# Optimization experiments

Measured on AMD Instinct MI355X. Metric: run time of the kernel, lower is better.

## Reference

```python
import jax, jax.numpy as jnp
import numpy as np

B, T, TM = 4, 1024, 1500
D_MODEL, D_FFN, H, D_HEAD, D_MEM = 1024, 4096, 16, 64, 1024
EPS = 1e-5


def layernorm(x, g):
    m = jnp.mean(x, axis=-1, keepdims=True)
    xc = x - m
    v = jnp.mean(xc * xc, axis=-1, keepdims=True)
    return xc * jax.lax.rsqrt(v + EPS) * g


def setup_inputs() -> dict:
    key = jax.random.key(0)
    ks = jax.random.split(key, 12)
    s = lambda fan_in: 1.0 / np.sqrt(fan_in)
    return {
        "x": jax.random.normal(ks[0], (B, T, D_MODEL), jnp.float32),
        "encoder_output": jax.random.normal(ks[1], (B, TM, D_MEM), jnp.float32),
        "encoder_mask": jax.random.randint(ks[2], (B, TM), 0, 2).astype(bool),
        "w_qkv": jax.random.normal(ks[3], (D_MODEL, 3 * H * D_HEAD), jnp.float32) * s(D_MODEL),
        "w_o_sa": jax.random.normal(ks[4], (H * D_HEAD, D_MODEL), jnp.float32) * s(H * D_HEAD),
        "w_q": jax.random.normal(ks[5], (D_MODEL, H * D_HEAD), jnp.float32) * s(D_MODEL),
        "w_kv": jax.random.normal(ks[6], (D_MEM, 2 * H * D_HEAD), jnp.float32) * s(D_MEM),
        "w_o_xa": jax.random.normal(ks[7], (H * D_HEAD, D_MODEL), jnp.float32) * s(H * D_HEAD),
        "w_ff1": jax.random.normal(ks[8], (D_MODEL, D_FFN), jnp.float32) * s(D_MODEL),
        "w_ff2": jax.random.normal(ks[9], (D_FFN, D_MODEL), jnp.float32) * s(D_FFN),
        "g_sa": jnp.ones((D_MODEL,), jnp.float32),
        "g_xaq": jnp.ones((D_MODEL,), jnp.float32),
        "g_xam": jnp.ones((D_MEM,), jnp.float32),
        "g_ff": jnp.ones((D_MODEL,), jnp.float32),
    }


def reference(x, encoder_output, encoder_mask, w_qkv, w_o_sa, w_q, w_kv, w_o_xa,
              w_ff1, w_ff2, g_sa, g_xaq, g_xam, g_ff):
    b, t, _ = x.shape
    scale = D_HEAD ** -0.5

    # ---- causal self-attention ----
    residual = x
    xn = layernorm(x, g_sa)
    qkv = (xn @ w_qkv).reshape(b, t, 3, H, D_HEAD)
    q, k, v = qkv[:, :, 0], qkv[:, :, 1], qkv[:, :, 2]  # (B,T,H,D)
    scores = jnp.einsum('bqhd,bkhd->bhqk', q, k) * scale
    causal = jnp.tril(jnp.ones((t, t), x.dtype))
    scores = scores + (1.0 - causal) * -1e9
    attn = jax.nn.softmax(scores, axis=-1)
    sa = jnp.einsum('bhqk,bkhd->bqhd', attn, v).reshape(b, t, H * D_HEAD)
    x = residual + sa @ w_o_sa

    # ---- cross-attention ----
    residual = x
    qn = layernorm(x, g_xaq)
    mn = layernorm(encoder_output, g_xam)
    tq, tm = t, mn.shape[1]
    qx = (qn @ w_q).reshape(b, tq, H, D_HEAD)
    kvx = (mn @ w_kv).reshape(b, tm, 2, H, D_HEAD)
    kx, vx = kvx[:, :, 0], kvx[:, :, 1]
    xs = jnp.einsum('bqhd,bkhd->bhqk', qx, kx) * scale
    xs = jnp.where(encoder_mask[:, None, None, :], xs, -jnp.inf)
    xattn = jax.nn.softmax(xs, axis=-1)
    xa = jnp.einsum('bhqk,bkhd->bqhd', xattn, vx).reshape(b, tq, H * D_HEAD)
    x = residual + xa @ w_o_xa

    # ---- pointwise FFN (kernel_size=1 conv == linear) ----
    residual = x
    h = layernorm(x, g_ff)
    h = jax.nn.gelu(h @ w_ff1, approximate=True) @ w_ff2
    x = residual + h
    return (x, k, v)
```

## Files before the change

### kernel.cpp

```cpp
#include <hip/hip_runtime.h>
#include <hip/hip_bf16.h>
#include <cstdint>
#include <cstddef>


typedef __attribute__((ext_vector_type(4))) float f32x4;
typedef __attribute__((ext_vector_type(8))) short s8v;
typedef __attribute__((ext_vector_type(2))) unsigned uint2v;

#define DEVI __device__ __forceinline__

DEVI short f2bf(float f) {
  union { float f; unsigned u; } x; x.f = f;
  unsigned r = x.u + 0x7fffu + ((x.u >> 16) & 1u);
  return (short)(r >> 16);
}
DEVI unsigned cvtpk_bf2(float lo, float hi) {
  unsigned r;
  asm("v_cvt_pk_bf16_f32 %0, %1, %2" : "=v"(r) : "v"(lo), "v"(hi));
  return r;
}
DEVI float fexp2(float x) {
  float r;
  asm("v_exp_f32 %0, %1" : "=v"(r) : "v"(x));
  return r;
}
DEVI float fmax3(float a, float b, float c) {
  float r;
  asm("v_max3_f32 %0, %1, %2, %3" : "=v"(r) : "v"(a), "v"(b), "v"(c));
  return r;
}
DEVI float bpermf(int srclane, float v) {
  union { float f; int i; } x; x.f = v;
  x.i = __builtin_amdgcn_ds_bpermute(srclane << 2, x.i);
  return x.f;
}
DEVI void gload_lds16(const void* g, void* l) {
  __builtin_amdgcn_global_load_lds((const __attribute__((address_space(1))) void*)g,
                                   (__attribute__((address_space(3))) void*)l,
                                   16, 0, 0);
}

DEVI void xcd_swizzle(int& bx, int& by) {
  int gx = gridDim.x, gy = gridDim.y;
  int nxy = gx * gy, chunk = nxy >> 3;
  int orig = blockIdx.y * gx + blockIdx.x;
  int gid = (orig & 7) * chunk + (orig >> 3);
  int full = gy << 3, nfull = gx >> 3, lim = nfull * full;
  if (gid < lim) {
    int band = gid / full, r = gid - band * full;
    bx = (band << 3) + (r & 7);
    by = r >> 3;
  } else {
    int r = gid - lim, w = gx - (nfull << 3);
    bx = (nfull << 3) + r % w;
    by = r / w;
  }
}

__global__ __launch_bounds__(256) void k_prep(
    const float* __restrict__ wqkv, const float* __restrict__ wosa,
    const float* __restrict__ wq,   const float* __restrict__ wkv,
    const float* __restrict__ woxa, const float* __restrict__ wff1,
    const float* __restrict__ wff2,
    short* __restrict__ wqkv_t, short* __restrict__ wosa_t,
    short* __restrict__ wq_t,   short* __restrict__ wkv_t,
    short* __restrict__ woxa_t, short* __restrict__ wff1_t,
    short* __restrict__ wff2_t,
    const int* __restrict__ mask, unsigned long long* __restrict__ mbits) {
  int id = blockIdx.x;
  const float* w; short* wt; int K, N, tx, r;
  if (id < 3072)       { w = wqkv; wt = wqkv_t; K = 1024; N = 3072; tx = 96;  r = id; }
  else if (id < 4096)  { w = wosa; wt = wosa_t; K = 1024; N = 1024; tx = 32;  r = id - 3072; }
  else if (id < 5120)  { w = wq;   wt = wq_t;   K = 1024; N = 1024; tx = 32;  r = id - 4096; }
  else if (id < 7168)  { w = wkv;  wt = wkv_t;  K = 1024; N = 2048; tx = 64;  r = id - 5120; }
  else if (id < 8192)  { w = woxa; wt = woxa_t; K = 1024; N = 1024; tx = 32;  r = id - 7168; }
  else if (id < 12288) { w = wff1; wt = wff1_t; K = 1024; N = 4096; tx = 128; r = id - 8192; }
  else if (id < 16384) { w = wff2; wt = wff2_t; K = 4096; N = 1024; tx = 32;  r = id - 12288; }
  else {
    int t = threadIdx.x;
    if (t < 96) {
      int b = t / 24, wd = t % 24;
      unsigned long long v = 0;
      const int* mb = mask + (size_t)b * 1500;
      for (int j = 0; j < 64; j++) {
        int k = wd * 64 + j;
        if (k < 1500 && mb[k]) v |= (1ull << j);
      }
      mbits[b * 24 + wd] = v;
    }
    return;
  }
  __shared__ float tile[32][33];
  int n0 = (r % tx) * 32, k0 = (r / tx) * 32;
  int t = threadIdx.x;
  int row = t >> 3, c4 = (t & 7) * 4;
  *(f32x4*)&tile[row][c4] = *(const f32x4*)(w + (size_t)(k0 + row) * N + n0 + c4);
  __syncthreads();
  float v0 = tile[c4 + 0][row], v1 = tile[c4 + 1][row];
  float v2 = tile[c4 + 2][row], v3 = tile[c4 + 3][row];
  uint2v o = {cvtpk_bf2(v0, v1), cvtpk_bf2(v2, v3)};
  *(uint2v*)(wt + (size_t)(n0 + row) * K + k0 + c4) = o;
}

__global__ __launch_bounds__(256) void k_vtrans(
    const short* __restrict__ src, int srs, int coff,
    short* __restrict__ dst, int T, int Tp) {
  __shared__ short tile[32][72];
  int bh = blockIdx.y, b = bh >> 4, h = bh & 15;
  int t0 = blockIdx.x * 32;
  const short* sB = src + (size_t)b * T * srs + coff + h * 64;
  short* dB = dst + (size_t)bh * 64 * Tp;
  int t = threadIdx.x;
  int r = t >> 3, c = (t & 7) * 8;
  int tr = t0 + r; if (tr > T - 1) tr = T - 1;
  *(s8v*)&tile[r][c] = *(const s8v*)(sB + (size_t)tr * srs + c);
  __syncthreads();
  int d = t & 63, ch = t >> 6;
  s8v o;
#pragma unroll
  for (int j = 0; j < 8; j++) o[j] = tile[ch * 8 + j][d];
  *(s8v*)(dB + (size_t)d * Tp + t0 + ch * 8) = o;
}

__global__ __launch_bounds__(256) void k_ln2(
    const float* __restrict__ x, const float* __restrict__ gx,
    short* __restrict__ ox,
    const float* __restrict__ e, const float* __restrict__ ge,
    short* __restrict__ oe) {
  int id = blockIdx.x;
  const float* src; const float* g; short* dst; int row;
  if (id < 4096) { src = x; g = gx; dst = ox; row = id; }
  else           { src = e; g = ge; dst = oe; row = id - 4096; }
  const float* xr = src + (size_t)row * 1024;
  int t = threadIdx.x, wid = t >> 6, lane = t & 63;
  f32x4 v = ((const f32x4*)xr)[t];
  float s = v[0] + v[1] + v[2] + v[3];
#pragma unroll
  for (int m = 32; m >= 1; m >>= 1) s += __shfl_xor(s, m);
  __shared__ float red[4];
  if (lane == 0) red[wid] = s;
  __syncthreads();
  float mean = (red[0] + red[1] + red[2] + red[3]) * (1.f / 1024.f);
  float q = 0.f;
#pragma unroll
  for (int i = 0; i < 4; i++) { v[i] -= mean; q += v[i] * v[i]; }
#pragma unroll
  for (int m = 32; m >= 1; m >>= 1) q += __shfl_xor(q, m);
  __syncthreads();
  if (lane == 0) red[wid] = q;
  __syncthreads();
  float var = (red[0] + red[1] + red[2] + red[3]) * (1.f / 1024.f);
  float rs = rsqrtf(var + 1e-5f);
  f32x4 gv = ((const f32x4*)g)[t];
  uint2v w = {cvtpk_bf2(v[0] * rs * gv[0], v[1] * rs * gv[1]),
              cvtpk_bf2(v[2] * rs * gv[2], v[3] * rs * gv[3])};
  *(uint2v*)(dst + (size_t)row * 1024 + t * 4) = w;
}

template <bool F32OUT, bool BF16OUT>
__global__ __launch_bounds__(256) void k_gemm3(
    const short* __restrict__ A, const short* __restrict__ Bt,
    float* __restrict__ Cf, short* __restrict__ Cb,
    int M, int N, int K, int lda, int ldb) {
  __shared__ short As[128 * 64];
  __shared__ short Bs[128 * 64];
  int z = blockIdx.z;
  A += (size_t)z * K;
  Bt += (size_t)z * K;
  if (F32OUT) Cf += (size_t)z * (size_t)M * N;

  int bx, by;
  xcd_swizzle(bx, by);
  int am = bx * 128, bn = by * 128;

  int t = threadIdx.x, wid = t >> 6, lane = t & 63;
  int la = lane & 15, lb = lane >> 4;
  int wr = wid >> 1, wc = wid & 1;

  const short* gp[8];
  int dof[8];
#pragma unroll
  for (int l = 0; l < 8; l++) {
    int cl = (l & 3) * 256 + t;
    int row = cl >> 3, g = cl & 7;
    int col = (g ^ (row & 7)) << 3;
    if (l < 4) {
      int ar = am + row; if (ar > M - 1) ar = M - 1;
      gp[l] = A + (size_t)ar * lda + col;
    } else {
      gp[l] = Bt + (size_t)(bn + row) * ldb + col;
    }
    dof[l] = ((l & 3) * 256 + wid * 64) * 8;
  }

  int aOff[4], bOff[4];
#pragma unroll
  for (int m = 0; m < 4; m++) {
    int r = wr * 64 + m * 16 + la;
    aOff[m] = r * 64 + ((lb ^ (r & 7)) << 3);
  }
#pragma unroll
  for (int n = 0; n < 4; n++) {
    int r = wc * 64 + n * 16 + la;
    bOff[n] = r * 64 + ((lb ^ (r & 7)) << 3);
  }

  f32x4 acc[4][4];
#pragma unroll
  for (int m = 0; m < 4; m++)
#pragma unroll
    for (int n = 0; n < 4; n++) acc[m][n] = (f32x4){0.f, 0.f, 0.f, 0.f};

  int nk = K >> 6;
  for (int ks = 0; ks < nk; ++ks) {
#pragma unroll
    for (int l = 0; l < 4; l++) { gload_lds16(gp[l], As + dof[l]); gp[l] += 64; }
#pragma unroll
    for (int l = 4; l < 8; l++) { gload_lds16(gp[l], Bs + dof[l]); gp[l] += 64; }
    __syncthreads();
#pragma unroll
    for (int kk = 0; kk < 2; kk++) {
      s8v af[4], bfg[4];
#pragma unroll
      for (int m = 0; m < 4; m++)
        af[m] = *(const s8v*)(As + (aOff[m] ^ (kk << 5)));
#pragma unroll
      for (int n = 0; n < 4; n++)
        bfg[n] = *(const s8v*)(Bs + (bOff[n] ^ (kk << 5)));
#pragma unroll
      for (int m = 0; m < 4; m++)
#pragma unroll
        for (int n = 0; n < 4; n++)
          acc[m][n] = __builtin_amdgcn_mfma_f32_16x16x32_bf16(af[m], bfg[n], acc[m][n], 0, 0, 0);
    }
    __syncthreads();
  }

#pragma unroll
  for (int m = 0; m < 4; m++) {
    int rb = am + wr * 64 + m * 16 + lb * 4;
#pragma unroll
    for (int n = 0; n < 4; n++) {
      int col = bn + wc * 64 + n * 16 + la;
#pragma unroll
      for (int j = 0; j < 4; j++) {
        int r = rb + j;
        if (r < M) {
          float v = acc[m][n][j];
          if (F32OUT) Cf[(size_t)r * N + col] = v;
          if (BF16OUT) Cb[(size_t)r * N + col] = f2bf(v);
        }
      }
    }
  }
}

template <bool GELU_, bool F32OUT, bool BF16OUT, bool KV>
__global__ __launch_bounds__(512) void k_gemm4(
    const short* __restrict__ A, const short* __restrict__ Bt,
    float* __restrict__ Cf, short* __restrict__ Cb,
    float* __restrict__ okv, int M, int N, int K, int lda, int ldb) {
  __shared__ short As[128 * 64];
  __shared__ short Bs[256 * 64];
  int z = blockIdx.z;
  A += (size_t)z * K;
  Bt += (size_t)z * K;
  if (F32OUT) Cf += (size_t)z * (size_t)M * N;

  int bx, by;
  xcd_swizzle(bx, by);
  int am = bx * 128, bn = by * 256;

  int t = threadIdx.x, wid = t >> 6, lane = t & 63;
  int la = lane & 15, lb = lane >> 4;
  int wr = wid >> 2, wc = wid & 3;

  const short* gpA[2]; const short* gpB[4];
  int dofA[2], dofB[4];
#pragma unroll
  for (int l = 0; l < 2; l++) {
    int c = l * 512 + t;
    int row = c >> 3, g = c & 7;
    int ar = am + row; if (ar > M - 1) ar = M - 1;
    gpA[l] = A + (size_t)ar * lda + ((g ^ (row & 7)) << 3);
    dofA[l] = (l * 512 + wid * 64) * 8;
  }
#pragma unroll
  for (int l = 0; l < 4; l++) {
    int c = l * 512 + t;
    int row = c >> 3, g = c & 7;
    gpB[l] = Bt + (size_t)(bn + row) * ldb + ((g ^ (row & 7)) << 3);
    dofB[l] = (l * 512 + wid * 64) * 8;
  }

  int aOff[4], bOff[4];
#pragma unroll
  for (int m = 0; m < 4; m++) {
    int r = wr * 64 + m * 16 + la;
    aOff[m] = r * 64 + ((lb ^ (r & 7)) << 3);
  }
#pragma unroll
  for (int n = 0; n < 4; n++) {
    int r = wc * 64 + n * 16 + la;
    bOff[n] = r * 64 + ((lb ^ (r & 7)) << 3);
  }

  f32x4 acc[4][4];
#pragma unroll
  for (int m = 0; m < 4; m++)
#pragma unroll
    for (int n = 0; n < 4; n++) acc[m][n] = (f32x4){0.f, 0.f, 0.f, 0.f};

  int nk = K >> 6;
  for (int ks = 0; ks < nk; ++ks) {
#pragma unroll
    for (int l = 0; l < 2; l++) { gload_lds16(gpA[l], As + dofA[l]); gpA[l] += 64; }
#pragma unroll
    for (int l = 0; l < 4; l++) { gload_lds16(gpB[l], Bs + dofB[l]); gpB[l] += 64; }
    __syncthreads();
#pragma unroll
    for (int kk = 0; kk < 2; kk++) {
      s8v af[4], bfg[4];
#pragma unroll
      for (int m = 0; m < 4; m++)
        af[m] = *(const s8v*)(As + (aOff[m] ^ (kk << 5)));
#pragma unroll
      for (int n = 0; n < 4; n++)
        bfg[n] = *(const s8v*)(Bs + (bOff[n] ^ (kk << 5)));
#pragma unroll
      for (int m = 0; m < 4; m++)
#pragma unroll
        for (int n = 0; n < 4; n++)
          acc[m][n] = __builtin_amdgcn_mfma_f32_16x16x32_bf16(af[m], bfg[n], acc[m][n], 0, 0, 0);
    }
    __syncthreads();
  }

#pragma unroll
  for (int m = 0; m < 4; m++) {
    int rb = am + wr * 64 + m * 16 + lb * 4;
#pragma unroll
    for (int n = 0; n < 4; n++) {
      int col = bn + wc * 64 + n * 16 + la;
#pragma unroll
      for (int j = 0; j < 4; j++) {
        int r = rb + j;
        if (r < M) {
          float v = acc[m][n][j];
          if (GELU_) {
            float u = v;
            float y = 0.7978845608f * u * (1.f + 0.044715f * u * u);
            float e = fexp2(fminf(y * 2.88539008f, 80.f));
            float th = (e - 1.f) * __builtin_amdgcn_rcpf(e + 1.f);
            v = 0.5f * u * (1.f + th);
          }
          if (F32OUT) Cf[(size_t)r * N + col] = v;
          if (BF16OUT) Cb[(size_t)r * N + col] = f2bf(v);
          if (KV) {
            if (col >= 2048)
              okv[(size_t)4096 * 1024 + (size_t)r * 1024 + (col - 2048)] = v;
            else if (col >= 1024)
              okv[(size_t)r * 1024 + (col - 1024)] = v;
          }
        }
      }
    }
  }
}

__global__ __launch_bounds__(256) void k_red2b(
    const f32x4* __restrict__ p, short* __restrict__ outb, int n) {
  int i = blockIdx.x * 256 + threadIdx.x;
  f32x4 v = p[i] + p[i + (size_t)n];
  uint2v w = {cvtpk_bf2(v[0], v[1]), cvtpk_bf2(v[2], v[3])};
  *(uint2v*)(outb + (size_t)i * 4) = w;
}

__global__ __launch_bounds__(256) void k_red4(
    const f32x4* __restrict__ p, const f32x4* __restrict__ res,
    float* __restrict__ outf, int n) {
  int i = blockIdx.x * 256 + threadIdx.x;
  f32x4 v = res[i] + ((p[i] + p[i + (size_t)n]) +
                      (p[i + 2 * (size_t)n] + p[i + 3 * (size_t)n]));
  ((f32x4*)outf)[i] = v;
}

__global__ __launch_bounds__(256) void k_red2ln(
    const f32x4* __restrict__ p, const f32x4* __restrict__ res,
    float* __restrict__ xout, short* __restrict__ nout,
    const float* __restrict__ g, int n) {
  int row = blockIdx.x;
  int t = threadIdx.x, wid = t >> 6, lane = t & 63;
  size_t i = (size_t)row * 256 + t;
  f32x4 v = res[i] + (p[i] + p[i + (size_t)n]);
  ((f32x4*)xout)[i] = v;
  float s = v[0] + v[1] + v[2] + v[3];
#pragma unroll
  for (int m = 32; m >= 1; m >>= 1) s += __shfl_xor(s, m);
  __shared__ float red[4];
  if (lane == 0) red[wid] = s;
  __syncthreads();
  float mean = (red[0] + red[1] + red[2] + red[3]) * (1.f / 1024.f);
  float q = 0.f;
#pragma unroll
  for (int k = 0; k < 4; k++) { v[k] -= mean; q += v[k] * v[k]; }
#pragma unroll
  for (int m = 32; m >= 1; m >>= 1) q += __shfl_xor(q, m);
  __syncthreads();
  if (lane == 0) red[wid] = q;
  __syncthreads();
  float var = (red[0] + red[1] + red[2] + red[3]) * (1.f / 1024.f);
  float rs = rsqrtf(var + 1e-5f);
  f32x4 gv = ((const f32x4*)g)[t];
  uint2v w = {cvtpk_bf2(v[0] * rs * gv[0], v[1] * rs * gv[1]),
              cvtpk_bf2(v[2] * rs * gv[2], v[3] * rs * gv[3])};
  *(uint2v*)(nout + (size_t)row * 1024 + t * 4) = w;
}

template <bool CAUSAL>
__global__ __launch_bounds__(512) void k_attn4(
    const short* __restrict__ qbuf, int qrs,
    const short* __restrict__ kbuf, int krs,
    const short* __restrict__ vT, int vts,
    short* __restrict__ obuf, int ors,
    const unsigned long long* __restrict__ mbits, int mwords,
    int Tq, int Tk, float scale) {
  __shared__ short Ks[64 * 64];
  __shared__ short Vs[64 * 64];
  __shared__ short Ps[8 * 1024];
  int lid = blockIdx.y * gridDim.x + blockIdx.x;
  int rest = lid >> 3;
  int bh = (lid & 7) * 8 + (rest & 7);
  int qsel = rest >> 3;
  int b = bh >> 4, h = bh & 15;
  int t = threadIdx.x, wid = t >> 6, lane = t & 63;
  int la = lane & 15, lb = lane >> 4;
  float lscale = scale * 1.44269504f;

  const short* qB = qbuf + (size_t)b * Tq * qrs + h * 64;
  const short* kB = kbuf + (size_t)b * Tk * krs + h * 64;
  const short* vB = vT + (size_t)bh * 64 * vts;
  char* Pw = (char*)(Ps + wid * 1024);

  int sr = t >> 3, scol = (t & 7) * 8;
  int swz = sr * 64 + (scol ^ ((sr & 7) << 3));

  int nsup = CAUSAL ? 2 : 1;
  for (int s = 0; s < nsup; s++) {
    int st = CAUSAL ? (s ? 7 - qsel : qsel) : qsel;
    int q0 = st * 128 + wid * 16;
    int nkt = CAUSAL ? 2 * st + 2 : (Tk + 63) >> 6;
    int lastkt = CAUSAL ? (q0 >> 6) : nkt - 1;

    s8v qf[2];
#pragma unroll
    for (int kk = 0; kk < 2; kk++)
      qf[kk] = *(const s8v*)(qB + (size_t)(q0 + la) * qrs + kk * 32 + lb * 8);

    f32x4 accO[4];
#pragma unroll
    for (int n = 0; n < 4; n++) accO[n] = (f32x4){0.f, 0.f, 0.f, 0.f};
    float m = -1e30f, l = 0.f;

    s8v krg, vrg;
    {
      int tk = sr; if (tk > Tk - 1) tk = Tk - 1;
      krg = *(const s8v*)(kB + (size_t)tk * krs + scol);
      vrg = *(const s8v*)(vB + (size_t)sr * vts + scol);
    }

    for (int kt = 0; kt < nkt; kt++) {
      int kb0 = kt << 6;
      __syncthreads();
      *(s8v*)&Ks[swz] = krg;
      *(s8v*)&Vs[swz] = vrg;
      __syncthreads();
      if (kt + 1 < nkt) {
        int kb = kb0 + 64;
        int tk = kb + sr; if (tk > Tk - 1) tk = Tk - 1;
        krg = *(const s8v*)(kB + (size_t)tk * krs + scol);
        vrg = *(const s8v*)(vB + (size_t)sr * vts + kb + scol);
      }
      if (kt > lastkt) continue;

      bool needMask;
      unsigned long long wm = ~0ull;
      if (CAUSAL) {
        needMask = (kt == lastkt);
      } else {
        wm = mbits[(size_t)b * mwords + kt];
        needMask = (wm != ~0ull);
      }

      float sc[4][4];
      __builtin_amdgcn_s_setprio(1);
#pragma unroll
      for (int n = 0; n < 4; n++) {
        f32x4 a = (f32x4){0.f, 0.f, 0.f, 0.f};
#pragma unroll
        for (int kk = 0; kk < 2; kk++) {
          s8v kf = *(const s8v*)&Ks[(n * 16 + la) * 64 +
                                    ((kk * 32 + lb * 8) ^ ((la & 7) << 3))];
          a = __builtin_amdgcn_mfma_f32_16x16x32_bf16(kf, qf[kk], a, 0, 0, 0);
        }
        if (needMask) {
#pragma unroll
          for (int j = 0; j < 4; j++) {
            int ki = n * 16 + lb * 4 + j;
            bool ok = CAUSAL ? (kb0 + ki <= q0 + la) : (((wm >> ki) & 1ull) != 0);
            sc[n][j] = ok ? a[j] : -1e30f;
          }
        } else {
#pragma unroll
          for (int j = 0; j < 4; j++) sc[n][j] = a[j];
        }
      }
      __builtin_amdgcn_s_setprio(0);

      float rn[4];
#pragma unroll
      for (int n = 0; n < 4; n++)
        rn[n] = fmaxf(fmax3(sc[n][0], sc[n][1], sc[n][2]), sc[n][3]);
      float tm = fmaxf(fmax3(rn[0], rn[1], rn[2]), rn[3]);
      tm = fmaxf(tm, __shfl_xor(tm, 16));
      tm = fmaxf(tm, __shfl_xor(tm, 32));
      tm = fmaxf(tm * lscale, -1e4f);

      bool skip = __all(tm - m <= 10.f);
      float alpha = 1.f;
      if (!skip) {
        float mn_ = fmaxf(m, tm);
        alpha = fexp2(m - mn_);
        m = mn_;
      }
      float nm = -m;

      unsigned W[4][2];
      float ps = 0.f;
#pragma unroll
      for (int n = 0; n < 4; n++) {
        float p0 = fexp2(__builtin_fmaf(sc[n][0], lscale, nm));
        float p1 = fexp2(__builtin_fmaf(sc[n][1], lscale, nm));
        float p2 = fexp2(__builtin_fmaf(sc[n][2], lscale, nm));
        float p3 = fexp2(__builtin_fmaf(sc[n][3], lscale, nm));
        ps += (p0 + p1) + (p2 + p3);
        W[n][0] = cvtpk_bf2(p0, p1);
        W[n][1] = cvtpk_bf2(p2, p3);
      }
      ps += __shfl_xor(ps, 16);
      ps += __shfl_xor(ps, 32);
      l = l * alpha + ps;

      if (!skip) {
#pragma unroll
        for (int j = 0; j < 4; j++) {
          float aj = bpermf(lb * 20 + j, alpha);
#pragma unroll
          for (int n = 0; n < 4; n++) accO[n][j] *= aj;
        }
      }

#pragma unroll
      for (int n = 0; n < 4; n++) {
        uint2v w2 = {W[n][0], W[n][1]};
        *(uint2v*)(Pw + ((la * 128 + n * 32 + lb * 8) ^ ((la & 7) << 4))) = w2;
      }
      __builtin_amdgcn_s_setprio(1);
#pragma unroll
      for (int kk = 0; kk < 2; kk++) {
        s8v pa = *(const s8v*)(Pw + ((la * 128 + kk * 64 + lb * 16) ^ ((la & 7) << 4)));
#pragma unroll
        for (int n = 0; n < 4; n++) {
          s8v vf = *(const s8v*)&Vs[(n * 16 + la) * 64 +
                                    ((kk * 32 + lb * 8) ^ ((la & 7) << 3))];
          accO[n] = __builtin_amdgcn_mfma_f32_16x16x32_bf16(pa, vf, accO[n], 0, 0, 0);
        }
      }
      __builtin_amdgcn_s_setprio(0);
    }

#pragma unroll
    for (int j = 0; j < 4; j++) {
      float lj = bpermf(lb * 20 + j, l);
      float inv = 1.f / lj;
      int r = q0 + lb * 4 + j;
#pragma unroll
      for (int n = 0; n < 4; n++)
        obuf[(size_t)(b * Tq + r) * ors + h * 64 + n * 16 + la] = f2bf(accO[n][j] * inv);
    }
  }
}

extern "C" void kernel_launch(void* const* d_in, const int* in_sizes, int n_in,
                              void* d_out, int out_size, void* d_ws, size_t ws_size,
                              hipStream_t stream) {
  (void)in_sizes; (void)n_in; (void)out_size; (void)ws_size;
  const float* x      = (const float*)d_in[0];
  const float* enc    = (const float*)d_in[1];
  const int*   mask   = (const int*)d_in[2];
  const float* w_qkv  = (const float*)d_in[3];
  const float* w_o_sa = (const float*)d_in[4];
  const float* w_q    = (const float*)d_in[5];
  const float* w_kv   = (const float*)d_in[6];
  const float* w_o_xa = (const float*)d_in[7];
  const float* w_ff1  = (const float*)d_in[8];
  const float* w_ff2  = (const float*)d_in[9];
  const float* g_sa   = (const float*)d_in[10];
  const float* g_xaq  = (const float*)d_in[11];
  const float* g_xam  = (const float*)d_in[12];
  const float* g_ff   = (const float*)d_in[13];

  float* out_x = (float*)d_out;
  float* out_k = out_x + (size_t)4096 * 1024;

  char* ws = (char*)d_ws;
  size_t off = 0;
  auto alloc = [&](size_t bytes) -> void* {
    void* p = ws + off;
    off += (bytes + 255) & ~(size_t)255;
    return p;
  };
  short* wqkv_t = (short*)alloc((size_t)3072 * 1024 * 2);
  short* wosa_t = (short*)alloc((size_t)1024 * 1024 * 2);
  short* wq_t   = (short*)alloc((size_t)1024 * 1024 * 2);
  short* wkv_t  = (short*)alloc((size_t)2048 * 1024 * 2);
  short* woxa_t = (short*)alloc((size_t)1024 * 1024 * 2);
  short* wff1_t = (short*)alloc((size_t)4096 * 1024 * 2);
  short* wff2_t = (short*)alloc((size_t)1024 * 4096 * 2);
  short* xn     = (short*)alloc((size_t)4096 * 1024 * 2);
  short* qkv_b  = (short*)alloc((size_t)4096 * 3072 * 2);
  short* sa_b   = (short*)alloc((size_t)4096 * 1024 * 2);
  float* x1     = (float*)alloc((size_t)4096 * 1024 * 4);
  short* qn     = (short*)alloc((size_t)4096 * 1024 * 2);
  short* mn     = (short*)alloc((size_t)6000 * 1024 * 2);
  short* qx_b   = (short*)alloc((size_t)4096 * 1024 * 2);
  short* kvx_b  = (short*)alloc((size_t)6000 * 2048 * 2);
  short* xa_b   = (short*)alloc((size_t)4096 * 1024 * 2);
  float* x2     = (float*)alloc((size_t)4096 * 1024 * 4);
  short* hn     = (short*)alloc((size_t)4096 * 1024 * 2);
  short* h1     = (short*)alloc((size_t)4096 * 4096 * 2);
  unsigned long long* mbits = (unsigned long long*)alloc(4 * 24 * 8);

  short* vTsa = xn;
  short* vTxa = h1;
  float* partH = (float*)h1;
  float* partQ = (float*)qkv_b;
  const int NRED = 1048576;

  k_prep<<<16385, 256, 0, stream>>>(
      w_qkv, w_o_sa, w_q, w_kv, w_o_xa, w_ff1, w_ff2,
      wqkv_t, wosa_t, wq_t, wkv_t, woxa_t, wff1_t, wff2_t, mask, mbits);
  k_ln2<<<10096, 256, 0, stream>>>(x, g_sa, xn, enc, g_xam, mn);

  k_gemm4<false, false, true, true><<<dim3(32, 12), 512, 0, stream>>>(
      xn, wqkv_t, nullptr, qkv_b, out_k, 4096, 3072, 1024, 1024, 1024);
  k_vtrans<<<dim3(32, 64), 256, 0, stream>>>(qkv_b, 3072, 2048, vTsa, 1024, 1024);
  k_attn4<true><<<dim3(4, 64), 512, 0, stream>>>(
      qkv_b, 3072, qkv_b + 1024, 3072, vTsa, 1024,
      sa_b, 1024, nullptr, 0, 1024, 1024, 0.125f);
  k_gemm3<true, false><<<dim3(32, 8, 2), 256, 0, stream>>>(
      sa_b, wosa_t, partH, nullptr, 4096, 1024, 512, 1024, 1024);
  k_red2ln<<<4096, 256, 0, stream>>>(
      (const f32x4*)partH, (const f32x4*)x, x1, qn, g_xaq, NRED);

  k_gemm3<true, false><<<dim3(32, 8, 2), 256, 0, stream>>>(
      qn, wq_t, partH, nullptr, 4096, 1024, 512, 1024, 1024);
  k_red2b<<<4096, 256, 0, stream>>>((const f32x4*)partH, qx_b, NRED);
  k_gemm4<false, false, true, false><<<dim3(47, 8), 512, 0, stream>>>(
      mn, wkv_t, nullptr, kvx_b, nullptr, 6000, 2048, 1024, 1024, 1024);
  k_vtrans<<<dim3(48, 64), 256, 0, stream>>>(kvx_b, 2048, 1024, vTxa, 1500, 1536);
  k_attn4<false><<<dim3(8, 64), 512, 0, stream>>>(
      qx_b, 1024, kvx_b, 2048, vTxa, 1536,
      xa_b, 1024, mbits, 24, 1024, 1500, 0.125f);
  k_gemm3<true, false><<<dim3(32, 8, 2), 256, 0, stream>>>(
      xa_b, woxa_t, partH, nullptr, 4096, 1024, 512, 1024, 1024);
  k_red2ln<<<4096, 256, 0, stream>>>(
      (const f32x4*)partH, (const f32x4*)x1, x2, hn, g_ff, NRED);

  k_gemm4<true, false, true, false><<<dim3(32, 16), 512, 0, stream>>>(
      hn, wff1_t, nullptr, h1, nullptr, 4096, 4096, 1024, 1024, 1024);
  k_gemm4<false, true, false, false><<<dim3(32, 4, 4), 512, 0, stream>>>(
      h1, wff2_t, partQ, nullptr, nullptr, 4096, 1024, 1024, 4096, 4096);
  k_red4<<<4096, 256, 0, stream>>>(
      (const f32x4*)partQ, (const f32x4*)x2, out_x, NRED);
}
```

Before: 385.2 us.

## Replace split-K GEMMs and reduction kernels with 128x64-tile GEMM fusing residual add

```diff
diff --git a/kernel.cpp b/kernel.cpp
--- a/kernel.cpp
+++ b/kernel.cpp
@@ -158,102 +158,34 @@
   *(uint2v*)(dst + (size_t)row * 1024 + t * 4) = w;
 }
 
-template <bool F32OUT, bool BF16OUT>
-__global__ __launch_bounds__(256) void k_gemm3(
-    const short* __restrict__ A, const short* __restrict__ Bt,
-    float* __restrict__ Cf, short* __restrict__ Cb,
-    int M, int N, int K, int lda, int ldb) {
-  __shared__ short As[128 * 64];
-  __shared__ short Bs[128 * 64];
-  int z = blockIdx.z;
-  A += (size_t)z * K;
-  Bt += (size_t)z * K;
-  if (F32OUT) Cf += (size_t)z * (size_t)M * N;
-
-  int bx, by;
-  xcd_swizzle(bx, by);
-  int am = bx * 128, bn = by * 128;
-
+__global__ __launch_bounds__(256) void k_ln(
+    const float* __restrict__ x, const float* __restrict__ g,
+    short* __restrict__ out) {
+  int row = blockIdx.x;
+  const float* xr = x + (size_t)row * 1024;
   int t = threadIdx.x, wid = t >> 6, lane = t & 63;
-  int la = lane & 15, lb = lane >> 4;
-  int wr = wid >> 1, wc = wid & 1;
-
-  const short* gp[8];
-  int dof[8];
-#pragma unroll
-  for (int l = 0; l < 8; l++) {
-    int cl = (l & 3) * 256 + t;
-    int row = cl >> 3, g = cl & 7;
-    int col = (g ^ (row & 7)) << 3;
-    if (l < 4) {
-      int ar = am + row; if (ar > M - 1) ar = M - 1;
-      gp[l] = A + (size_t)ar * lda + col;
-    } else {
-      gp[l] = Bt + (size_t)(bn + row) * ldb + col;
-    }
-    dof[l] = ((l & 3) * 256 + wid * 64) * 8;
-  }
-
-  int aOff[4], bOff[4];
-#pragma unroll
-  for (int m = 0; m < 4; m++) {
-    int r = wr * 64 + m * 16 + la;
-    aOff[m] = r * 64 + ((lb ^ (r & 7)) << 3);
-  }
-#pragma unroll
-  for (int n = 0; n < 4; n++) {
-    int r = wc * 64 + n * 16 + la;
-    bOff[n] = r * 64 + ((lb ^ (r & 7)) << 3);
-  }
-
-  f32x4 acc[4][4];
-#pragma unroll
-  for (int m = 0; m < 4; m++)
-#pragma unroll
-    for (int n = 0; n < 4; n++) acc[m][n] = (f32x4){0.f, 0.f, 0.f, 0.f};
-
-  int nk = K >> 6;
-  for (int ks = 0; ks < nk; ++ks) {
-#pragma unroll
-    for (int l = 0; l < 4; l++) { gload_lds16(gp[l], As + dof[l]); gp[l] += 64; }
-#pragma unroll
-    for (int l = 4; l < 8; l++) { gload_lds16(gp[l], Bs + dof[l]); gp[l] += 64; }
-    __syncthreads();
-#pragma unroll
-    for (int kk = 0; kk < 2; kk++) {
-      s8v af[4], bfg[4];
-#pragma unroll
-      for (int m = 0; m < 4; m++)
-        af[m] = *(const s8v*)(As + (aOff[m] ^ (kk << 5)));
-#pragma unroll
-      for (int n = 0; n < 4; n++)
-        bfg[n] = *(const s8v*)(Bs + (bOff[n] ^ (kk << 5)));
-#pragma unroll
-      for (int m = 0; m < 4; m++)
-#pragma unroll
-        for (int n = 0; n < 4; n++)
-          acc[m][n] = __builtin_amdgcn_mfma_f32_16x16x32_bf16(af[m], bfg[n], acc[m][n], 0, 0, 0);
-    }
-    __syncthreads();
-  }
-
-#pragma unroll
-  for (int m = 0; m < 4; m++) {
-    int rb = am + wr * 64 + m * 16 + lb * 4;
-#pragma unroll
-    for (int n = 0; n < 4; n++) {
-      int col = bn + wc * 64 + n * 16 + la;
-#pragma unroll
-      for (int j = 0; j < 4; j++) {
-        int r = rb + j;
-        if (r < M) {
-          float v = acc[m][n][j];
-          if (F32OUT) Cf[(size_t)r * N + col] = v;
-          if (BF16OUT) Cb[(size_t)r * N + col] = f2bf(v);
-        }
-      }
-    }
-  }
+  f32x4 v = ((const f32x4*)xr)[t];
+  float s = v[0] + v[1] + v[2] + v[3];
+#pragma unroll
+  for (int m = 32; m >= 1; m >>= 1) s += __shfl_xor(s, m);
+  __shared__ float red[4];
+  if (lane == 0) red[wid] = s;
+  __syncthreads();
+  float mean = (red[0] + red[1] + red[2] + red[3]) * (1.f / 1024.f);
+  float q = 0.f;
+#pragma unroll
+  for (int i = 0; i < 4; i++) { v[i] -= mean; q += v[i] * v[i]; }
+#pragma unroll
+  for (int m = 32; m >= 1; m >>= 1) q += __shfl_xor(q, m);
+  __syncthreads();
+  if (lane == 0) red[wid] = q;
+  __syncthreads();
+  float var = (red[0] + red[1] + red[2] + red[3]) * (1.f / 1024.f);
+  float rs = rsqrtf(var + 1e-5f);
+  f32x4 gv = ((const f32x4*)g)[t];
+  uint2v w = {cvtpk_bf2(v[0] * rs * gv[0], v[1] * rs * gv[1]),
+              cvtpk_bf2(v[2] * rs * gv[2], v[3] * rs * gv[3])};
+  *(uint2v*)(out + (size_t)row * 1024 + t * 4) = w;
 }
 
 template <bool GELU_, bool F32OUT, bool BF16OUT, bool KV>
@@ -263,10 +195,6 @@
     float* __restrict__ okv, int M, int N, int K, int lda, int ldb) {
   __shared__ short As[128 * 64];
   __shared__ short Bs[256 * 64];
-  int z = blockIdx.z;
-  A += (size_t)z * K;
-  Bt += (size_t)z * K;
-  if (F32OUT) Cf += (size_t)z * (size_t)M * N;
 
   int bx, by;
   xcd_swizzle(bx, by);
@@ -369,53 +297,101 @@
   }
 }
 
-__global__ __launch_bounds__(256) void k_red2b(
-    const f32x4* __restrict__ p, short* __restrict__ outb, int n) {
-  int i = blockIdx.x * 256 + threadIdx.x;
-  f32x4 v = p[i] + p[i + (size_t)n];
-  uint2v w = {cvtpk_bf2(v[0], v[1]), cvtpk_bf2(v[2], v[3])};
-  *(uint2v*)(outb + (size_t)i * 4) = w;
-}
-
-__global__ __launch_bounds__(256) void k_red4(
-    const f32x4* __restrict__ p, const f32x4* __restrict__ res,
-    float* __restrict__ outf, int n) {
-  int i = blockIdx.x * 256 + threadIdx.x;
-  f32x4 v = res[i] + ((p[i] + p[i + (size_t)n]) +
-                      (p[i + 2 * (size_t)n] + p[i + 3 * (size_t)n]));
-  ((f32x4*)outf)[i] = v;
-}
-
-__global__ __launch_bounds__(256) void k_red2ln(
-    const f32x4* __restrict__ p, const f32x4* __restrict__ res,
-    float* __restrict__ xout, short* __restrict__ nout,
-    const float* __restrict__ g, int n) {
-  int row = blockIdx.x;
+template <bool RES, bool F32OUT, bool BF16OUT>
+__global__ __launch_bounds__(256) void k_gemm5(
+    const short* __restrict__ A, const short* __restrict__ Bt,
+    float* __restrict__ Cf, short* __restrict__ Cb,
+    const float* __restrict__ res, int M, int N, int K, int lda, int ldb) {
+  __shared__ short As[128 * 64];
+  __shared__ short Bs[64 * 64];
+
+  int bx, by;
+  xcd_swizzle(bx, by);
+  int am = bx * 128, bn = by * 64;
+
   int t = threadIdx.x, wid = t >> 6, lane = t & 63;
-  size_t i = (size_t)row * 256 + t;
-  f32x4 v = res[i] + (p[i] + p[i + (size_t)n]);
-  ((f32x4*)xout)[i] = v;
-  float s = v[0] + v[1] + v[2] + v[3];
-#pragma unroll
-  for (int m = 32; m >= 1; m >>= 1) s += __shfl_xor(s, m);
-  __shared__ float red[4];
-  if (lane == 0) red[wid] = s;
-  __syncthreads();
-  float mean = (red[0] + red[1] + red[2] + red[3]) * (1.f / 1024.f);
-  float q = 0.f;
-#pragma unroll
-  for (int k = 0; k < 4; k++) { v[k] -= mean; q += v[k] * v[k]; }
-#pragma unroll
-  for (int m = 32; m >= 1; m >>= 1) q += __shfl_xor(q, m);
-  __syncthreads();
-  if (lane == 0) red[wid] = q;
-  __syncthreads();
-  float var = (red[0] + red[1] + red[2] + red[3]) * (1.f / 1024.f);
-  float rs = rsqrtf(var + 1e-5f);
-  f32x4 gv = ((const f32x4*)g)[t];
-  uint2v w = {cvtpk_bf2(v[0] * rs * gv[0], v[1] * rs * gv[1]),
-              cvtpk_bf2(v[2] * rs * gv[2], v[3] * rs * gv[3])};
-  *(uint2v*)(nout + (size_t)row * 1024 + t * 4) = w;
+  int la = lane & 15, lb = lane >> 4;
+  int wr = wid >> 1, wc = wid & 1;
+
+  const short* gpA[4]; const short* gpB[2];
+  int dofA[4], dofB[2];
+#pragma unroll
+  for (int l = 0; l < 4; l++) {
+    int cl = l * 256 + t;
+    int row = cl >> 3, g = cl & 7;
+    int ar = am + row; if (ar > M - 1) ar = M - 1;
+    gpA[l] = A + (size_t)ar * lda + ((g ^ (row & 7)) << 3);
+    dofA[l] = (l * 256 + wid * 64) * 8;
+  }
+#pragma unroll
+  for (int l = 0; l < 2; l++) {
+    int cl = l * 256 + t;
+    int row = cl >> 3, g = cl & 7;
+    gpB[l] = Bt + (size_t)(bn + row) * ldb + ((g ^ (row & 7)) << 3);
+    dofB[l] = (l * 256 + wid * 64) * 8;
+  }
+
+  int aOff[4], bOff[2];
+#pragma unroll
+  for (int m = 0; m < 4; m++) {
+    int r = wr * 64 + m * 16 + la;
+    aOff[m] = r * 64 + ((lb ^ (r & 7)) << 3);
+  }
+#pragma unroll
+  for (int n = 0; n < 2; n++) {
+    int r = wc * 32 + n * 16 + la;
+    bOff[n] = r * 64 + ((lb ^ (r & 7)) << 3);
+  }
+
+  f32x4 acc[4][2];
+#pragma unroll
+  for (int m = 0; m < 4; m++)
+#pragma unroll
+    for (int n = 0; n < 2; n++) acc[m][n] = (f32x4){0.f, 0.f, 0.f, 0.f};
+
+  int nk = K >> 6;
+  for (int ks = 0; ks < nk; ++ks) {
+#pragma unroll
+    for (int l = 0; l < 4; l++) { gload_lds16(gpA[l], As + dofA[l]); gpA[l] += 64; }
+#pragma unroll
+    for (int l = 0; l < 2; l++) { gload_lds16(gpB[l], Bs + dofB[l]); gpB[l] += 64; }
+    __syncthreads();
+#pragma unroll
+    for (int kk = 0; kk < 2; kk++) {
+      s8v af[4], bfg[2];
+#pragma unroll
+      for (int m = 0; m < 4; m++)
+        af[m] = *(const s8v*)(As + (aOff[m] ^ (kk << 5)));
+#pragma unroll
+      for (int n = 0; n < 2; n++)
+        bfg[n] = *(const s8v*)(Bs + (bOff[n] ^ (kk << 5)));
+#pragma unroll
+      for (int m = 0; m < 4; m++)
+#pragma unroll
+        for (int n = 0; n < 2; n++)
+          acc[m][n] = __builtin_amdgcn_mfma_f32_16x16x32_bf16(af[m], bfg[n], acc[m][n], 0, 0, 0);
+    }
+    __syncthreads();
+  }
+
+#pragma unroll
+  for (int m = 0; m < 4; m++) {
+    int rb = am + wr * 64 + m * 16 + lb * 4;
+#pragma unroll
+    for (int n = 0; n < 2; n++) {
+      int col = bn + wc * 32 + n * 16 + la;
+#pragma unroll
+      for (int j = 0; j < 4; j++) {
+        int r = rb + j;
+        if (r < M) {
+          float v = acc[m][n][j];
+          if (RES) v += res[(size_t)r * N + col];
+          if (F32OUT) Cf[(size_t)r * N + col] = v;
+          if (BF16OUT) Cb[(size_t)r * N + col] = f2bf(v);
+        }
+      }
+    }
+  }
 }
 
 template <bool CAUSAL>
@@ -433,6 +409,7 @@
   int rest = lid >> 3;
   int bh = (lid & 7) * 8 + (rest & 7);
   int qsel = rest >> 3;
+  int st = CAUSAL ? (7 - qsel) : qsel;
   int b = bh >> 4, h = bh & 15;
   int t = threadIdx.x, wid = t >> 6, lane = t & 63;
   int la = lane & 15, lb = lane >> 4;
@@ -446,149 +423,145 @@
   int sr = t >> 3, scol = (t & 7) * 8;
   int swz = sr * 64 + (scol ^ ((sr & 7) << 3));
 
-  int nsup = CAUSAL ? 2 : 1;
-  for (int s = 0; s < nsup; s++) {
-    int st = CAUSAL ? (s ? 7 - qsel : qsel) : qsel;
-    int q0 = st * 128 + wid * 16;
-    int nkt = CAUSAL ? 2 * st + 2 : (Tk + 63) >> 6;
-    int lastkt = CAUSAL ? (q0 >> 6) : nkt - 1;
-
-    s8v qf[2];
-#pragma unroll
-    for (int kk = 0; kk < 2; kk++)
-      qf[kk] = *(const s8v*)(qB + (size_t)(q0 + la) * qrs + kk * 32 + lb * 8);
-
-    f32x4 accO[4];
-#pragma unroll
-    for (int n = 0; n < 4; n++) accO[n] = (f32x4){0.f, 0.f, 0.f, 0.f};
-    float m = -1e30f, l = 0.f;
-
-    s8v krg, vrg;
-    {
-      int tk = sr; if (tk > Tk - 1) tk = Tk - 1;
+  int q0 = st * 128 + wid * 16;
+  int nkt = CAUSAL ? 2 * st + 2 : (Tk + 63) >> 6;
+  int lastkt = CAUSAL ? (q0 >> 6) : nkt - 1;
+
+  s8v qf[2];
+#pragma unroll
+  for (int kk = 0; kk < 2; kk++)
+    qf[kk] = *(const s8v*)(qB + (size_t)(q0 + la) * qrs + kk * 32 + lb * 8);
+
+  f32x4 accO[4];
+#pragma unroll
+  for (int n = 0; n < 4; n++) accO[n] = (f32x4){0.f, 0.f, 0.f, 0.f};
+  float m = -1e30f, l = 0.f;
+
+  s8v krg, vrg;
+  {
+    int tk = sr; if (tk > Tk - 1) tk = Tk - 1;
+    krg = *(const s8v*)(kB + (size_t)tk * krs + scol);
+    vrg = *(const s8v*)(vB + (size_t)sr * vts + scol);
+  }
+
+  for (int kt = 0; kt < nkt; kt++) {
+    int kb0 = kt << 6;
+    __syncthreads();
+    *(s8v*)&Ks[swz] = krg;
+    *(s8v*)&Vs[swz] = vrg;
+    __syncthreads();
+    if (kt + 1 < nkt) {
+      int kb = kb0 + 64;
+      int tk = kb + sr; if (tk > Tk - 1) tk = Tk - 1;
       krg = *(const s8v*)(kB + (size_t)tk * krs + scol);
-      vrg = *(const s8v*)(vB + (size_t)sr * vts + scol);
-    }
-
-    for (int kt = 0; kt < nkt; kt++) {
-      int kb0 = kt << 6;
-      __syncthreads();
-      *(s8v*)&Ks[swz] = krg;
-      *(s8v*)&Vs[swz] = vrg;
-      __syncthreads();
-      if (kt + 1 < nkt) {
-        int kb = kb0 + 64;
-        int tk = kb + sr; if (tk > Tk - 1) tk = Tk - 1;
-        krg = *(const s8v*)(kB + (size_t)tk * krs + scol);
-        vrg = *(const s8v*)(vB + (size_t)sr * vts + kb + scol);
+      vrg = *(const s8v*)(vB + (size_t)sr * vts + kb + scol);
+    }
+    if (kt > lastkt) continue;
+
+    bool needMask;
+    unsigned long long wm = ~0ull;
+    if (CAUSAL) {
+      needMask = (kt == lastkt);
+    } else {
+      wm = mbits[(size_t)b * mwords + kt];
+      needMask = (wm != ~0ull);
+    }
+
+    float sc[4][4];
+    __builtin_amdgcn_s_setprio(1);
+#pragma unroll
+    for (int n = 0; n < 4; n++) {
+      f32x4 a = (f32x4){0.f, 0.f, 0.f, 0.f};
+#pragma unroll
+      for (int kk = 0; kk < 2; kk++) {
+        s8v kf = *(const s8v*)&Ks[(n * 16 + la) * 64 +
+                                  ((kk * 32 + lb * 8) ^ ((la & 7) << 3))];
+        a = __builtin_amdgcn_mfma_f32_16x16x32_bf16(kf, qf[kk], a, 0, 0, 0);
       }
-      if (kt > lastkt) continue;
-
-      bool needMask;
-      unsigned long long wm = ~0ull;
-      if (CAUSAL) {
-        needMask = (kt == lastkt);
+      if (needMask) {
+#pragma unroll
+        for (int j = 0; j < 4; j++) {
+          int ki = n * 16 + lb * 4 + j;
+          bool ok = CAUSAL ? (kb0 + ki <= q0 + la) : (((wm >> ki) & 1ull) != 0);
+          sc[n][j] = ok ? a[j] : -1e30f;
+        }
       } else {
-        wm = mbits[(size_t)b * mwords + kt];
-        needMask = (wm != ~0ull);
+#pragma unroll
+        for (int j = 0; j < 4; j++) sc[n][j] = a[j];
       }
-
-      float sc[4][4];
-      __builtin_amdgcn_s_setprio(1);
+    }
+    __builtin_amdgcn_s_setprio(0);
+
+    float rn[4];
+#pragma unroll
+    for (int n = 0; n < 4; n++)
+      rn[n] = fmaxf(fmax3(sc[n][0], sc[n][1], sc[n][2]), sc[n][3]);
+    float tm = fmaxf(fmax3(rn[0], rn[1], rn[2]), rn[3]);
+    tm = fmaxf(tm, __shfl_xor(tm, 16));
+    tm = fmaxf(tm, __shfl_xor(tm, 32));
+    tm = fmaxf(tm * lscale, -1e4f);
+
+    bool skip = __all(tm - m <= 10.f);
+    float alpha = 1.f;
+    if (!skip) {
+      float mn_ = fmaxf(m, tm);
+      alpha = fexp2(m - mn_);
+      m = mn_;
+    }
+    float nm = -m;
+
+    unsigned W[4][2];
+    float ps = 0.f;
+#pragma unroll
+    for (int n = 0; n < 4; n++) {
+      float p0 = fexp2(__builtin_fmaf(sc[n][0], lscale, nm));
+      float p1 = fexp2(__builtin_fmaf(sc[n][1], lscale, nm));
+      float p2 = fexp2(__builtin_fmaf(sc[n][2], lscale, nm));
+      float p3 = fexp2(__builtin_fmaf(sc[n][3], lscale, nm));
+      ps += (p0 + p1) + (p2 + p3);
+      W[n][0] = cvtpk_bf2(p0, p1);
+      W[n][1] = cvtpk_bf2(p2, p3);
+    }
+    ps += __shfl_xor(ps, 16);
+    ps += __shfl_xor(ps, 32);
+    l = l * alpha + ps;
+
+    if (!skip) {
+#pragma unroll
+      for (int j = 0; j < 4; j++) {
+        float aj = bpermf(lb * 20 + j, alpha);
+#pragma unroll
+        for (int n = 0; n < 4; n++) accO[n][j] *= aj;
+      }
+    }
+
+#pragma unroll
+    for (int n = 0; n < 4; n++) {
+      uint2v w2 = {W[n][0], W[n][1]};
+      *(uint2v*)(Pw + ((la * 128 + n * 32 + lb * 8) ^ ((la & 7) << 4))) = w2;
+    }
+    __builtin_amdgcn_s_setprio(1);
+#pragma unroll
+    for (int kk = 0; kk < 2; kk++) {
+      s8v pa = *(const s8v*)(Pw + ((la * 128 + kk * 64 + lb * 16) ^ ((la & 7) << 4)));
 #pragma unroll
       for (int n = 0; n < 4; n++) {
-        f32x4 a = (f32x4){0.f, 0.f, 0.f, 0.f};
-#pragma unroll
-        for (int kk = 0; kk < 2; kk++) {
-          s8v kf = *(const s8v*)&Ks[(n * 16 + la) * 64 +
-                                    ((kk * 32 + lb * 8) ^ ((la & 7) << 3))];
-          a = __builtin_amdgcn_mfma_f32_16x16x32_bf16(kf, qf[kk], a, 0, 0, 0);
-        }
-        if (needMask) {
-#pragma unroll
-          for (int j = 0; j < 4; j++) {
-            int ki = n * 16 + lb * 4 + j;
-            bool ok = CAUSAL ? (kb0 + ki <= q0 + la) : (((wm >> ki) & 1ull) != 0);
-            sc[n][j] = ok ? a[j] : -1e30f;
-          }
-        } else {
-#pragma unroll
-          for (int j = 0; j < 4; j++) sc[n][j] = a[j];
-        }
+        s8v vf = *(const s8v*)&Vs[(n * 16 + la) * 64 +
+                                  ((kk * 32 + lb * 8) ^ ((la & 7) << 3))];
+        accO[n] = __builtin_amdgcn_mfma_f32_16x16x32_bf16(pa, vf, accO[n], 0, 0, 0);
       }
-      __builtin_amdgcn_s_setprio(0);
-
-      float rn[4];
-#pragma unroll
-      for (int n = 0; n < 4; n++)
-        rn[n] = fmaxf(fmax3(sc[n][0], sc[n][1], sc[n][2]), sc[n][3]);
-      float tm = fmaxf(fmax3(rn[0], rn[1], rn[2]), rn[3]);
-      tm = fmaxf(tm, __shfl_xor(tm, 16));
-      tm = fmaxf(tm, __shfl_xor(tm, 32));
-      tm = fmaxf(tm * lscale, -1e4f);
-
-      bool skip = __all(tm - m <= 10.f);
-      float alpha = 1.f;
-      if (!skip) {
-        float mn_ = fmaxf(m, tm);
-        alpha = fexp2(m - mn_);
-        m = mn_;
-      }
-      float nm = -m;
-
-      unsigned W[4][2];
-      float ps = 0.f;
-#pragma unroll
-      for (int n = 0; n < 4; n++) {
-        float p0 = fexp2(__builtin_fmaf(sc[n][0], lscale, nm));
-        float p1 = fexp2(__builtin_fmaf(sc[n][1], lscale, nm));
-        float p2 = fexp2(__builtin_fmaf(sc[n][2], lscale, nm));
-        float p3 = fexp2(__builtin_fmaf(sc[n][3], lscale, nm));
-        ps += (p0 + p1) + (p2 + p3);
-        W[n][0] = cvtpk_bf2(p0, p1);
-        W[n][1] = cvtpk_bf2(p2, p3);
-      }
-      ps += __shfl_xor(ps, 16);
-      ps += __shfl_xor(ps, 32);
-      l = l * alpha + ps;
-
-      if (!skip) {
-#pragma unroll
-        for (int j = 0; j < 4; j++) {
-          float aj = bpermf(lb * 20 + j, alpha);
-#pragma unroll
-          for (int n = 0; n < 4; n++) accO[n][j] *= aj;
-        }
-      }
-
-#pragma unroll
-      for (int n = 0; n < 4; n++) {
-        uint2v w2 = {W[n][0], W[n][1]};
-        *(uint2v*)(Pw + ((la * 128 + n * 32 + lb * 8) ^ ((la & 7) << 4))) = w2;
-      }
-      __builtin_amdgcn_s_setprio(1);
-#pragma unroll
-      for (int kk = 0; kk < 2; kk++) {
-        s8v pa = *(const s8v*)(Pw + ((la * 128 + kk * 64 + lb * 16) ^ ((la & 7) << 4)));
-#pragma unroll
-        for (int n = 0; n < 4; n++) {
-          s8v vf = *(const s8v*)&Vs[(n * 16 + la) * 64 +
-                                    ((kk * 32 + lb * 8) ^ ((la & 7) << 3))];
-          accO[n] = __builtin_amdgcn_mfma_f32_16x16x32_bf16(pa, vf, accO[n], 0, 0, 0);
-        }
-      }
-      __builtin_amdgcn_s_setprio(0);
-    }
-
-#pragma unroll
-    for (int j = 0; j < 4; j++) {
-      float lj = bpermf(lb * 20 + j, l);
-      float inv = 1.f / lj;
-      int r = q0 + lb * 4 + j;
-#pragma unroll
-      for (int n = 0; n < 4; n++)
-        obuf[(size_t)(b * Tq + r) * ors + h * 64 + n * 16 + la] = f2bf(accO[n][j] * inv);
-    }
+    }
+    __builtin_amdgcn_s_setprio(0);
+  }
+
+#pragma unroll
+  for (int j = 0; j < 4; j++) {
+    float lj = bpermf(lb * 20 + j, l);
+    float inv = 1.f / lj;
+    int r = q0 + lb * 4 + j;
+#pragma unroll
+    for (int n = 0; n < 4; n++)
+      obuf[(size_t)(b * Tq + r) * ors + h * 64 + n * 16 + la] = f2bf(accO[n][j] * inv);
   }
 }
 
@@ -644,9 +617,6 @@
 
   short* vTsa = xn;
   short* vTxa = h1;
-  float* partH = (float*)h1;
-  float* partQ = (float*)qkv_b;
-  const int NRED = 1048576;
 
   k_prep<<<16385, 256, 0, stream>>>(
       w_qkv, w_o_sa, w_q, w_kv, w_o_xa, w_ff1, w_ff2,
@@ -656,32 +626,27 @@
   k_gemm4<false, false, true, true><<<dim3(32, 12), 512, 0, stream>>>(
       xn, wqkv_t, nullptr, qkv_b, out_k, 4096, 3072, 1024, 1024, 1024);
   k_vtrans<<<dim3(32, 64), 256, 0, stream>>>(qkv_b, 3072, 2048, vTsa, 1024, 1024);
-  k_attn4<true><<<dim3(4, 64), 512, 0, stream>>>(
+  k_attn4<true><<<dim3(8, 64), 512, 0, stream>>>(
       qkv_b, 3072, qkv_b + 1024, 3072, vTsa, 1024,
       sa_b, 1024, nullptr, 0, 1024, 1024, 0.125f);
-  k_gemm3<true, false><<<dim3(32, 8, 2), 256, 0, stream>>>(
-      sa_b, wosa_t, partH, nullptr, 4096, 1024, 512, 1024, 1024);
-  k_red2ln<<<4096, 256, 0, stream>>>(
-      (const f32x4*)partH, (const f32x4*)x, x1, qn, g_xaq, NRED);
-
-  k_gemm3<true, false><<<dim3(32, 8, 2), 256, 0, stream>>>(
-      qn, wq_t, partH, nullptr, 4096, 1024, 512, 1024, 1024);
-  k_red2b<<<4096, 256, 0, stream>>>((const f32x4*)partH, qx_b, NRED);
+  k_gemm5<true, true, false><<<dim3(32, 16), 256, 0, stream>>>(
+      sa_b, wosa_t, x1, nullptr, x, 4096, 1024, 1024, 1024, 1024);
+  k_ln<<<4096, 256, 0, stream>>>(x1, g_xaq, qn);
+
+  k_gemm5<false, false, true><<<dim3(32, 16), 256, 0, stream>>>(
+      qn, wq_t, nullptr, qx_b, nullptr, 4096, 1024, 1024, 1024, 1024);
   k_gemm4<false, false, true, false><<<dim3(47, 8), 512, 0, stream>>>(
       mn, wkv_t, nullptr, kvx_b, nullptr, 6000, 2048, 1024, 1024, 1024);
   k_vtrans<<<dim3(48, 64), 256, 0, stream>>>(kvx_b, 2048, 1024, vTxa, 1500, 1536);
   k_attn4<false><<<dim3(8, 64), 512, 0, stream>>>(
       qx_b, 1024, kvx_b, 2048, vTxa, 1536,
       xa_b, 1024, mbits, 24, 1024, 1500, 0.125f);
-  k_gemm3<true, false><<<dim3(32, 8, 2), 256, 0, stream>>>(
-      xa_b, woxa_t, partH, nullptr, 4096, 1024, 512, 1024, 1024);
-  k_red2ln<<<4096, 256, 0, stream>>>(
-      (const f32x4*)partH, (const f32x4*)x1, x2, hn, g_ff, NRED);
+  k_gemm5<true, true, false><<<dim3(32, 16), 256, 0, stream>>>(
+      xa_b, woxa_t, x2, nullptr, x1, 4096, 1024, 1024, 1024, 1024);
+  k_ln<<<4096, 256, 0, stream>>>(x2, g_ff, hn);
 
   k_gemm4<true, false, true, false><<<dim3(32, 16), 512, 0, stream>>>(
       hn, wff1_t, nullptr, h1, nullptr, 4096, 4096, 1024, 1024, 1024);
-  k_gemm4<false, true, false, false><<<dim3(32, 4, 4), 512, 0, stream>>>(
-      h1, wff2_t, partQ, nullptr, nullptr, 4096, 1024, 1024, 4096, 4096);
-  k_red4<<<4096, 256, 0, stream>>>(
-      (const f32x4*)partQ, (const f32x4*)x2, out_x, NRED);
-}
+  k_gemm5<true, true, false><<<dim3(32, 16), 256, 0, stream>>>(
+      h1, wff2_t, out_x, nullptr, x2, 4096, 1024, 4096, 4096, 4096);
+}
```

New measurement: 387.6 us. No clear change (+0.6%).
